# Kernel tuning notes

Hardware: AMD Instinct MI355X
Metric: run time of the kernel (lower is better)

## Reference

```python
import jax, jax.numpy as jnp
import numpy as np

B = 64            # number of graphs in the batch
D = 128           # in_node_dim
NUM_VIEWS = 4
MAX_NODES = 508   # max(node_counts) for the deterministic counts below


def _make_counts():
    # deterministic ragged node counts: 256, 260, ..., 508
    return jnp.asarray(256 + 4 * np.arange(B), dtype=jnp.int64)


def setup_inputs() -> dict:
    key = jax.random.key(0)
    node_counts = _make_counts()
    total = int(np.sum(256 + 4 * np.arange(B)))  # 24448
    z_nodes = jax.random.normal(key, (total, D), dtype=jnp.float32)
    return {"z_nodes": z_nodes, "node_counts": node_counts}


def reference(z_nodes, node_counts):
    # Pad ragged node embeddings into a dense [B, MAX_NODES, D] block with
    # zero rows for padding; then padded z @ z^T directly equals the
    # zero-padded per-graph adjacency logits (outer products with zero rows
    # are zero), matching the torch loop + torch.zeros pad.
    offsets = jnp.concatenate([jnp.zeros((1,), node_counts.dtype),
                               jnp.cumsum(node_counts)[:-1]])          # [B]
    pos = jnp.arange(MAX_NODES)                                        # [M]
    valid = pos[None, :] < node_counts[:, None]                        # [B, M]
    idx = jnp.where(valid, offsets[:, None] + pos[None, :], 0)         # [B, M]
    z_pad = z_nodes[idx] * valid[..., None].astype(z_nodes.dtype)      # [B, M, D]
    adj = jnp.einsum('bnd,bmd->bnm', z_pad, z_pad)                     # [B, M, M]
    # unsqueeze(1).repeat(1, V, 1, 1)
    return jnp.broadcast_to(adj[:, None], (B, NUM_VIEWS, MAX_NODES, MAX_NODES))
```

## Files before the change

### kernel.cpp

```cpp
#include <hip/hip_runtime.h>
#include <stdint.h>


typedef __bf16          v8bf __attribute__((ext_vector_type(8)));
typedef unsigned short  v8us __attribute__((ext_vector_type(8)));
typedef float           v4f  __attribute__((ext_vector_type(4)));
typedef unsigned int    v4u  __attribute__((ext_vector_type(4)));

#define NMAX  508
#define DD    128
#define NV    4
#define IMG   (NMAX * NMAX)
#define IMGV4 (IMG / 4)
#define ROWV4 (NMAX / 4)
#define LDS2  516

__device__ __forceinline__ unsigned short f32_to_bf16_rne(float f) {
    unsigned int u = __builtin_bit_cast(unsigned int, f);
    u = (u + 0x7fffu + ((u >> 16) & 1u)) >> 16;
    return (unsigned short)u;
}

__device__ __forceinline__ v8bf cvt8(v4f lo, v4f hi) {
    v8us u;
    u[0] = f32_to_bf16_rne(lo.x); u[1] = f32_to_bf16_rne(lo.y);
    u[2] = f32_to_bf16_rne(lo.z); u[3] = f32_to_bf16_rne(lo.w);
    u[4] = f32_to_bf16_rne(hi.x); u[5] = f32_to_bf16_rne(hi.y);
    u[6] = f32_to_bf16_rne(hi.z); u[7] = f32_to_bf16_rne(hi.w);
    return __builtin_bit_cast(v8bf, u);
}

__global__ __launch_bounds__(256, 4)
void adj_gram_kernel(const float* __restrict__ z,
                     const int*   __restrict__ counts,
                     float*       __restrict__ out)
{
    __shared__ __align__(16) float sC[16 * LDS2];

    const int blk = blockIdx.x;
    const int b   = blk >> 5;
    const int sl  = blk & 31;
    const int i0  = sl * 16;

    const int tid  = threadIdx.x;
    const int lane = tid & 63;
    const int wave = tid >> 6;
    const int j0   = wave * 128;

    const bool is64 = (counts[1] == 0);
    int cnt = is64 ? counts[2 * lane] : counts[lane];
    int inc = cnt;
    #pragma unroll
    for (int s = 1; s < 64; s <<= 1) {
        int t = __shfl_up(inc, s);
        if (lane >= s) inc += t;
    }
    const int n   = __shfl(cnt, b);
    const int off = __shfl(inc, b) - n;

    const int lr = lane & 15;
    const int lk = (lane >> 4) * 8;

    v4f acc[8];
    #pragma unroll
    for (int nt = 0; nt < 8; ++nt) acc[nt] = (v4f)0.0f;

    if (i0 < n) {
        const float* zb = z + (size_t)off * DD;
        #pragma unroll
        for (int ks = 0; ks < 4; ++ks) {
            const int ko = ks * 32 + lk;
            v8bf af, bfv[8];
            {
                const int r = i0 + lr;
                v4f lo = (v4f)0.0f, hi = (v4f)0.0f;
                if (r < n) {
                    const float* p = zb + (size_t)r * DD + ko;
                    lo = *(const v4f*)p;
                    hi = *(const v4f*)(p + 4);
                }
                af = cvt8(lo, hi);
            }
            #pragma unroll
            for (int nt = 0; nt < 8; ++nt) {
                const int r = j0 + nt * 16 + lr;
                v4f lo = (v4f)0.0f, hi = (v4f)0.0f;
                if (r < n) {
                    const float* p = zb + (size_t)r * DD + ko;
                    lo = *(const v4f*)p;
                    hi = *(const v4f*)(p + 4);
                }
                bfv[nt] = cvt8(lo, hi);
            }
            #pragma unroll
            for (int nt = 0; nt < 8; ++nt)
                acc[nt] = __builtin_amdgcn_mfma_f32_16x16x32_bf16(
                    af, bfv[nt], acc[nt], 0, 0, 0);
        }
    }

    const int crow = (lane >> 4) * 4;
    #pragma unroll
    for (int nt = 0; nt < 8; ++nt)
        #pragma unroll
        for (int rr = 0; rr < 4; ++rr)
            sC[(crow + rr) * LDS2 + j0 + nt * 16 + lr] = acc[nt][rr];
    __syncthreads();

    const int rowsv = (NMAX - i0 < 16) ? (NMAX - i0) : 16;
    const int nvec  = rowsv * ROWV4;
    for (int v = 0; v < NV; ++v) {
        const size_t G0 = (size_t)(b * NV + v) * IMGV4 + (size_t)i0 * ROWV4;
        const size_t Ga = G0 & ~(size_t)7;
        const size_t G1 = G0 + (size_t)nvec;
        for (size_t g = Ga + tid; g < G1; g += 256) {
            if (g < G0) continue;
            const int f   = (int)(g - G0);
            const int row = f / ROWV4;
            const int c4  = f - row * ROWV4;
            const v4u val = *(const v4u*)&sC[row * LDS2 + c4 * 4];
            *(v4u*)(out + g * 4) = val;
        }
    }
}

extern "C" void kernel_launch(void* const* d_in, const int* in_sizes, int n_in,
                              void* d_out, int out_size, void* d_ws, size_t ws_size,
                              hipStream_t stream) {
    const float* z      = (const float*)d_in[0];
    const int*   counts = (const int*)d_in[1];
    float*       out    = (float*)d_out;
    adj_gram_kernel<<<dim3(64 * 32), dim3(256), 0, stream>>>(z, counts, out);
}
```

Measured before the change: 295.3 us.

## Precompute bf16 k-chunk-major copy of z in workspace and swizzle block order

```diff
diff --git a/kernel.cpp b/kernel.cpp
--- a/kernel.cpp
+++ b/kernel.cpp
@@ -10,6 +10,7 @@
 #define NMAX  508
 #define DD    128
 #define NV    4
+#define TOTAL 24448
 #define IMG   (NMAX * NMAX)
 #define IMGV4 (IMG / 4)
 #define ROWV4 (NMAX / 4)
@@ -21,26 +22,39 @@
     return (unsigned short)u;
 }
 
-__device__ __forceinline__ v8bf cvt8(v4f lo, v4f hi) {
+__device__ __forceinline__ v8us pack8(v4f lo, v4f hi) {
     v8us u;
     u[0] = f32_to_bf16_rne(lo.x); u[1] = f32_to_bf16_rne(lo.y);
     u[2] = f32_to_bf16_rne(lo.z); u[3] = f32_to_bf16_rne(lo.w);
     u[4] = f32_to_bf16_rne(hi.x); u[5] = f32_to_bf16_rne(hi.y);
     u[6] = f32_to_bf16_rne(hi.z); u[7] = f32_to_bf16_rne(hi.w);
-    return __builtin_bit_cast(v8bf, u);
+    return u;
+}
+
+__global__ __launch_bounds__(256)
+void cvt_transpose_kernel(const float* __restrict__ z,
+                          unsigned short* __restrict__ zt)
+{
+    const int r   = blockIdx.x * 256 + threadIdx.x;
+    const int koi = blockIdx.y;
+    if (r >= TOTAL) return;
+    const float* p = z + (size_t)r * DD + koi * 8;
+    const v4f lo = *(const v4f*)p;
+    const v4f hi = *(const v4f*)(p + 4);
+    *(v8us*)(zt + ((size_t)koi * TOTAL + r) * 8) = pack8(lo, hi);
 }
 
 __global__ __launch_bounds__(256, 4)
-void adj_gram_kernel(const float* __restrict__ z,
-                     const int*   __restrict__ counts,
-                     float*       __restrict__ out)
+void adj_gram_zt_kernel(const unsigned short* __restrict__ zt,
+                        const int* __restrict__ counts,
+                        float* __restrict__ out)
 {
     __shared__ __align__(16) float sC[16 * LDS2];
 
-    const int blk = blockIdx.x;
-    const int b   = blk >> 5;
-    const int sl  = blk & 31;
-    const int i0  = sl * 16;
+    const int blk  = blockIdx.x;
+    const int wgid = (blk & 7) * 256 + (blk >> 3);
+    const int b    = wgid >> 5;
+    const int i0   = (wgid & 31) * 16;
 
     const int tid  = threadIdx.x;
     const int lane = tid & 63;
@@ -59,38 +73,28 @@
     const int off = __shfl(inc, b) - n;
 
     const int lr = lane & 15;
-    const int lk = (lane >> 4) * 8;
+    const int lg = lane >> 4;
 
     v4f acc[8];
     #pragma unroll
     for (int nt = 0; nt < 8; ++nt) acc[nt] = (v4f)0.0f;
 
     if (i0 < n) {
-        const float* zb = z + (size_t)off * DD;
         #pragma unroll
         for (int ks = 0; ks < 4; ++ks) {
-            const int ko = ks * 32 + lk;
+            const int koi = ks * 4 + lg;
+            const unsigned short* pl = zt + (size_t)koi * TOTAL * 8;
             v8bf af, bfv[8];
             {
                 const int r = i0 + lr;
-                v4f lo = (v4f)0.0f, hi = (v4f)0.0f;
-                if (r < n) {
-                    const float* p = zb + (size_t)r * DD + ko;
-                    lo = *(const v4f*)p;
-                    hi = *(const v4f*)(p + 4);
-                }
-                af = cvt8(lo, hi);
+                af = (r < n) ? *(const v8bf*)(pl + (size_t)(off + r) * 8)
+                             : (v8bf)(__bf16)0.0f;
             }
             #pragma unroll
             for (int nt = 0; nt < 8; ++nt) {
                 const int r = j0 + nt * 16 + lr;
-                v4f lo = (v4f)0.0f, hi = (v4f)0.0f;
-                if (r < n) {
-                    const float* p = zb + (size_t)r * DD + ko;
-                    lo = *(const v4f*)p;
-                    hi = *(const v4f*)(p + 4);
-                }
-                bfv[nt] = cvt8(lo, hi);
+                bfv[nt] = (r < n) ? *(const v8bf*)(pl + (size_t)(off + r) * 8)
+                                  : (v8bf)(__bf16)0.0f;
             }
             #pragma unroll
             for (int nt = 0; nt < 8; ++nt)
@@ -99,7 +103,7 @@
         }
     }
 
-    const int crow = (lane >> 4) * 4;
+    const int crow = lg * 4;
     #pragma unroll
     for (int nt = 0; nt < 8; ++nt)
         #pragma unroll
@@ -118,8 +122,89 @@
             const int f   = (int)(g - G0);
             const int row = f / ROWV4;
             const int c4  = f - row * ROWV4;
-            const v4u val = *(const v4u*)&sC[row * LDS2 + c4 * 4];
-            *(v4u*)(out + g * 4) = val;
+            *(v4u*)(out + g * 4) = *(const v4u*)&sC[row * LDS2 + c4 * 4];
+        }
+    }
+}
+
+__global__ __launch_bounds__(256, 4)
+void adj_gram_fb_kernel(const float* __restrict__ z,
+                        const int*   __restrict__ counts,
+                        float*       __restrict__ out)
+{
+    __shared__ __align__(16) float sC[16 * LDS2];
+    const int blk = blockIdx.x;
+    const int b   = blk >> 5;
+    const int i0  = (blk & 31) * 16;
+    const int tid  = threadIdx.x;
+    const int lane = tid & 63;
+    const int wave = tid >> 6;
+    const int j0   = wave * 128;
+    const bool is64 = (counts[1] == 0);
+    int cnt = is64 ? counts[2 * lane] : counts[lane];
+    int inc = cnt;
+    #pragma unroll
+    for (int s = 1; s < 64; s <<= 1) {
+        int t = __shfl_up(inc, s);
+        if (lane >= s) inc += t;
+    }
+    const int n   = __shfl(cnt, b);
+    const int off = __shfl(inc, b) - n;
+    const int lr = lane & 15;
+    const int lk = (lane >> 4) * 8;
+    v4f acc[8];
+    #pragma unroll
+    for (int nt = 0; nt < 8; ++nt) acc[nt] = (v4f)0.0f;
+    if (i0 < n) {
+        const float* zb = z + (size_t)off * DD;
+        #pragma unroll
+        for (int ks = 0; ks < 4; ++ks) {
+            const int ko = ks * 32 + lk;
+            v8bf af, bfv[8];
+            {
+                const int r = i0 + lr;
+                v4f lo = (v4f)0.0f, hi = (v4f)0.0f;
+                if (r < n) {
+                    const float* p = zb + (size_t)r * DD + ko;
+                    lo = *(const v4f*)p; hi = *(const v4f*)(p + 4);
+                }
+                af = __builtin_bit_cast(v8bf, pack8(lo, hi));
+            }
+            #pragma unroll
+            for (int nt = 0; nt < 8; ++nt) {
+                const int r = j0 + nt * 16 + lr;
+                v4f lo = (v4f)0.0f, hi = (v4f)0.0f;
+                if (r < n) {
+                    const float* p = zb + (size_t)r * DD + ko;
+                    lo = *(const v4f*)p; hi = *(const v4f*)(p + 4);
+                }
+                bfv[nt] = __builtin_bit_cast(v8bf, pack8(lo, hi));
+            }
+            #pragma unroll
+            for (int nt = 0; nt < 8; ++nt)
+                acc[nt] = __builtin_amdgcn_mfma_f32_16x16x32_bf16(
+                    af, bfv[nt], acc[nt], 0, 0, 0);
+        }
+    }
+    const int crow = (lane >> 4) * 4;
+    #pragma unroll
+    for (int nt = 0; nt < 8; ++nt)
+        #pragma unroll
+        for (int rr = 0; rr < 4; ++rr)
+            sC[(crow + rr) * LDS2 + j0 + nt * 16 + lr] = acc[nt][rr];
+    __syncthreads();
+    const int rowsv = (NMAX - i0 < 16) ? (NMAX - i0) : 16;
+    const int nvec  = rowsv * ROWV4;
+    for (int v = 0; v < NV; ++v) {
+        const size_t G0 = (size_t)(b * NV + v) * IMGV4 + (size_t)i0 * ROWV4;
+        const size_t Ga = G0 & ~(size_t)7;
+        const size_t G1 = G0 + (size_t)nvec;
+        for (size_t g = Ga + tid; g < G1; g += 256) {
+            if (g < G0) continue;
+            const int f   = (int)(g - G0);
+            const int row = f / ROWV4;
+            const int c4  = f - row * ROWV4;
+            *(v4u*)(out + g * 4) = *(const v4u*)&sC[row * LDS2 + c4 * 4];
         }
     }
 }
@@ -130,5 +215,14 @@
     const float* z      = (const float*)d_in[0];
     const int*   counts = (const int*)d_in[1];
     float*       out    = (float*)d_out;
-    adj_gram_kernel<<<dim3(64 * 32), dim3(256), 0, stream>>>(z, counts, out);
-}
+    const size_t need   = (size_t)TOTAL * 16 * 16;
+
+    if (d_ws != nullptr && ws_size >= need) {
+        unsigned short* zt = (unsigned short*)d_ws;
+        cvt_transpose_kernel<<<dim3((TOTAL + 255) / 256, 16), dim3(256), 0, stream>>>(
+            z, zt);
+        adj_gram_zt_kernel<<<dim3(64 * 32), dim3(256), 0, stream>>>(zt, counts, out);
+    } else {
+        adj_gram_fb_kernel<<<dim3(64 * 32), dim3(256), 0, stream>>>(z, counts, out);
+    }
+}
```

Result: faster. 271.0 us (-8.2%).
